# Kernel optimization log

Hardware: AMD Instinct MI355X
Metric: run time of the kernel (lower is better)

## Reference

```python
import jax, jax.numpy as jnp
import numpy as np

D_MODEL = 1024
N_HEADS = 2
D_FF = 4096
SEQ = 4096
HEAD_DIM = D_MODEL // N_HEADS
SCALE = HEAD_DIM ** 0.5
LN_EPS = 1e-5


def _layer_norm(x, g, b):
    mu = jnp.mean(x, axis=-1, keepdims=True)
    var = jnp.mean(jnp.square(x - mu), axis=-1, keepdims=True)
    return (x - mu) * jax.lax.rsqrt(var + LN_EPS) * g + b


def _gelu_tanh(x):
    # torch nn.GELU(approximate='tanh')
    c = np.sqrt(2.0 / np.pi).astype(np.float32)
    return 0.5 * x * (1.0 + jnp.tanh(c * (x + 0.044715 * x * x * x)))


def setup_inputs() -> dict:
    key = jax.random.key(0)
    ks = jax.random.split(key, 12)
    s = 1.0 / np.sqrt(D_MODEL)
    sf = 1.0 / np.sqrt(D_FF)
    inp = {
        "x": jax.random.normal(ks[0], (SEQ, D_MODEL), jnp.float32),
        "ln1_g": jnp.ones((D_MODEL,), jnp.float32),
        "ln1_b": jnp.zeros((D_MODEL,), jnp.float32),
        "wq": jax.random.normal(ks[1], (D_MODEL, D_MODEL), jnp.float32) * s,
        "bq": jnp.zeros((D_MODEL,), jnp.float32),
        "wk": jax.random.normal(ks[2], (D_MODEL, D_MODEL), jnp.float32) * s,
        "bk": jnp.zeros((D_MODEL,), jnp.float32),
        "wv": jax.random.normal(ks[3], (D_MODEL, D_MODEL), jnp.float32) * s,
        "bv": jnp.zeros((D_MODEL,), jnp.float32),
        "wo": jax.random.normal(ks[4], (D_MODEL, D_MODEL), jnp.float32) * s,
        "bo": jnp.zeros((D_MODEL,), jnp.float32),
        "ln2_g": jnp.ones((D_MODEL,), jnp.float32),
        "ln2_b": jnp.zeros((D_MODEL,), jnp.float32),
        "w1": jax.random.normal(ks[5], (D_FF, D_MODEL), jnp.float32) * s,
        "b1": jnp.zeros((D_FF,), jnp.float32),
        "w2": jax.random.normal(ks[6], (D_MODEL, D_FF), jnp.float32) * sf,
        "b2": jnp.zeros((D_MODEL,), jnp.float32),
    }
    return inp


def reference(x, ln1_g, ln1_b, wq, bq, wk, bk, wv, bv, wo, bo,
              ln2_g, ln2_b, w1, b1, w2, b2):
    S = x.shape[0]
    h = _layer_norm(x, ln1_g, ln1_b)
    # torch Linear: y = h @ W.T + b
    q = h @ wq.T + bq
    k = h @ wk.T + bk
    v = h @ wv.T + bv
    # chunk(2, dim=-1) == reshape last dim to (heads, head_dim)
    qh = q.reshape(S, N_HEADS, HEAD_DIM)
    kh = k.reshape(S, N_HEADS, HEAD_DIM)
    vh = v.reshape(S, N_HEADS, HEAD_DIM)
    scores = jnp.einsum('shd,thd->hst', qh, kh) / SCALE  # [H,S,S]
    attn = jax.nn.softmax(scores, axis=-1)
    o = jnp.einsum('hst,thd->shd', attn, vh).reshape(S, D_MODEL)
    x = x + (o @ wo.T + bo)
    h2 = _layer_norm(x, ln2_g, ln2_b)
    ff = _gelu_tanh(h2 @ w1.T + b1) @ w2.T + b2
    return x + ff
```

## Files before the change

kernel.cpp:

```cpp
#include <hip/hip_runtime.h>
#include <math.h>

#define SEQ 4096
#define DM  1024
#define DFF 4096
#define NH  2
#define HD  512

typedef unsigned short ushort_t;
typedef short  s16x8 __attribute__((ext_vector_type(8)));
typedef float  f32x4 __attribute__((ext_vector_type(4)));
typedef unsigned short u16x8 __attribute__((ext_vector_type(8)));

__device__ __forceinline__ float bf2f(unsigned short u) {
    return __uint_as_float(((unsigned)u) << 16);
}
__device__ __forceinline__ unsigned short f2bf(float f) {
    unsigned u = __float_as_uint(f);
    unsigned r = (u + 0x7fffu + ((u >> 16) & 1u)) >> 16;
    return (unsigned short)r;
}

__device__ __forceinline__ void async_load16(void* lds, const void* g) {
    __builtin_amdgcn_global_load_lds(
        (const __attribute__((address_space(1))) void*)g,
        (__attribute__((address_space(3))) void*)lds, 16, 0, 0);
}

template<bool HAS_BIAS, bool DO_GELU, bool HAS_RES, bool OUT_BF16, int SPLITS,
         int MODE, int BM, bool TRV>
__global__ __launch_bounds__(BM == 256 ? 512 : 256)
void gemm_nt(const ushort_t* __restrict__ A, int lda,
             const ushort_t* __restrict__ B, int ldb,
             void* __restrict__ Cv, int ldc,
             const float* __restrict__ bias,
             const float* __restrict__ res, int ldres,
             int K, float alpha,
             size_t strA, size_t strB, size_t strC, size_t strBias,
             float* __restrict__ rowsum, ushort_t* __restrict__ vt)
{
    __shared__ alignas(16) ushort_t sA[BM * 64];
    __shared__ alignas(16) ushort_t sB[128 * 64];

    const int z  = blockIdx.z;
    const int zb = z / SPLITS;
    const int ks = (z % SPLITS) * K;
    A += (size_t)zb * strA;
    B += (size_t)zb * strB;
    if (HAS_BIAS) bias += (size_t)zb * strBias;

    const int tid   = threadIdx.x;
    const int lane  = tid & 63;
    const int wave  = tid >> 6;
    const int waveM = wave >> 1, waveN = wave & 1;
    const int m0 = blockIdx.y * BM, n0 = blockIdx.x * 128;
    const int lr = lane & 15, quad = lane >> 4;

    f32x4 acc[4][4] = {};

    const ushort_t* Ag = A + (size_t)m0 * lda + ks;
    const ushort_t* Bg = B + (size_t)n0 * ldb + ks;

    const int ldRow = (lane >> 3);
    const int ldCol = (((lane & 7) ^ (lane >> 3)) * 8);
    const int NB = (BM == 256) ? 2 : 4;
    const int BW = (BM == 256) ? 16 : 32;

    for (int k0 = 0; k0 < K; k0 += 64) {
#pragma unroll
        for (int i = 0; i < 4; ++i) {
            int r = wave * 32 + i * 8 + ldRow;
            async_load16(&sA[(wave * 32 + i * 8) * 64],
                         Ag + (size_t)r * lda + k0 + ldCol);
        }
#pragma unroll
        for (int i = 0; i < NB; ++i) {
            int r = wave * BW + i * 8 + ldRow;
            async_load16(&sB[(wave * BW + i * 8) * 64],
                         Bg + (size_t)r * ldb + k0 + ldCol);
        }
        __syncthreads();

#pragma unroll
        for (int kk = 0; kk < 64; kk += 32) {
            const int pg = ((((kk >> 3) + quad) ^ (lr & 7)) << 3);
            s16x8 af[4], bfr[4];
#pragma unroll
            for (int mi = 0; mi < 4; ++mi)
                af[mi] = *(const s16x8*)&sA[(waveM * 64 + mi * 16 + lr) * 64 + pg];
#pragma unroll
            for (int ni = 0; ni < 4; ++ni)
                bfr[ni] = *(const s16x8*)&sB[(waveN * 64 + ni * 16 + lr) * 64 + pg];
#pragma unroll
            for (int mi = 0; mi < 4; ++mi)
#pragma unroll
                for (int ni = 0; ni < 4; ++ni)
                    acc[mi][ni] = __builtin_amdgcn_mfma_f32_16x16x32_bf16(
                        af[mi], bfr[ni], acc[mi][ni], 0, 0, 0);
        }
        __syncthreads();
    }

    if (TRV && zb == 2) {
#pragma unroll
        for (int mi = 0; mi < 4; ++mi) {
#pragma unroll
            for (int ni = 0; ni < 4; ++ni) {
                int t0 = m0 + waveM * 64 + mi * 16 + quad * 4;
                int col = n0 + waveN * 64 + ni * 16 + lr;
                unsigned b[4];
#pragma unroll
                for (int r = 0; r < 4; ++r) {
                    float v = acc[mi][ni][r] * alpha;
                    if (HAS_BIAS) v += bias[col];
                    b[r] = f2bf(v);
                }
                uint2 pk;
                pk.x = b[0] | (b[1] << 16);
                pk.y = b[2] | (b[3] << 16);
                int h = col >> 9, d = col & (HD - 1);
                *(uint2*)(vt + (size_t)h * HD * SEQ + (size_t)d * SEQ + t0) = pk;
            }
        }
        return;
    }

    float rs_part[4][4];
    if (MODE == 1) {
#pragma unroll
        for (int mi = 0; mi < 4; ++mi)
#pragma unroll
            for (int r = 0; r < 4; ++r) rs_part[mi][r] = 0.0f;
    }

#pragma unroll
    for (int mi = 0; mi < 4; ++mi) {
#pragma unroll
        for (int r = 0; r < 4; ++r) {
            int row = m0 + waveM * 64 + mi * 16 + quad * 4 + r;
#pragma unroll
            for (int ni = 0; ni < 4; ++ni) {
                int col = n0 + waveN * 64 + ni * 16 + lr;
                float v = acc[mi][ni][r] * alpha;
                if (HAS_BIAS) v += bias[col];
                if (DO_GELU) {
                    float xx = v;
                    float y2 = 1.5957691216057308f * (xx + 0.044715f * xx * xx * xx);
                    float t = __expf(y2);
                    v = xx * t / (t + 1.0f);
                }
                if (HAS_RES) v += res[(size_t)row * ldres + col];
                if (OUT_BF16) {
                    ushort_t bs = f2bf(MODE == 1 ? __expf(v) : v);
                    if (MODE == 1) rs_part[mi][r] += bf2f(bs);
                    ((ushort_t*)Cv)[(size_t)z * strC + (size_t)row * ldc + col] = bs;
                } else {
                    ((float*)Cv)[(size_t)z * strC + (size_t)row * ldc + col] = v;
                }
            }
        }
    }

    if (MODE == 1) {
#pragma unroll
        for (int mi = 0; mi < 4; ++mi) {
#pragma unroll
            for (int r = 0; r < 4; ++r) {
                float s = rs_part[mi][r];
                s += __shfl_xor(s, 1);
                s += __shfl_xor(s, 2);
                s += __shfl_xor(s, 4);
                s += __shfl_xor(s, 8);
                if (lr == 0) {
                    int row = m0 + waveM * 64 + mi * 16 + quad * 4 + r;
                    atomicAdd(&rowsum[(size_t)zb * SEQ + row], s);
                }
            }
        }
    }
}

template<int S, bool HAS_BIAS, bool HAS_RES, bool OUT_BF16, bool DIV_RS>
__global__ __launch_bounds__(256)
void reduce_splitk(const float* __restrict__ P, size_t slab,
                   void* __restrict__ outv, int N, int ldout, int colStride,
                   const float* __restrict__ bias,
                   const float* __restrict__ res, int ldres,
                   const float* __restrict__ rowsum)
{
    const int z = blockIdx.z;
    const float* Pz = P + (size_t)z * S * slab;
    size_t i = ((size_t)blockIdx.x * 256 + threadIdx.x) * 4;
    if (i >= slab) return;
    int row = (int)(i / (size_t)N);
    int col = (int)(i - (size_t)row * N);
    float4 a = *(const float4*)(Pz + i);
#pragma unroll
    for (int s = 1; s < S; ++s) {
        float4 b = *(const float4*)(Pz + (size_t)s * slab + i);
        a.x += b.x; a.y += b.y; a.z += b.z; a.w += b.w;
    }
    if (DIV_RS) {
        float inv = 1.0f / rowsum[(size_t)z * SEQ + row];
        a.x *= inv; a.y *= inv; a.z *= inv; a.w *= inv;
    }
    int oc = z * colStride + col;
    if (HAS_BIAS) {
        a.x += bias[oc]; a.y += bias[oc + 1]; a.z += bias[oc + 2]; a.w += bias[oc + 3];
    }
    if (HAS_RES) {
        float4 r4 = *(const float4*)(res + (size_t)row * ldres + oc);
        a.x += r4.x; a.y += r4.y; a.z += r4.z; a.w += r4.w;
    }
    if (OUT_BF16) {
        ushort_t* o = (ushort_t*)outv + (size_t)row * ldout + oc;
        o[0] = f2bf(a.x); o[1] = f2bf(a.y); o[2] = f2bf(a.z); o[3] = f2bf(a.w);
    } else {
        *(float4*)((float*)outv + (size_t)row * ldout + oc) = a;
    }
}

__global__ __launch_bounds__(256)
void reduce_oproj_ln(const float* __restrict__ P,
                     const float* __restrict__ bo, const float* __restrict__ x,
                     float* __restrict__ X1,
                     const float* __restrict__ g, const float* __restrict__ b,
                     ushort_t* __restrict__ H)
{
    int row = blockIdx.x;
    int tid = threadIdx.x;
    size_t off = (size_t)row * DM + tid * 4;
    float4 p0 = *(const float4*)(P + off);
    float4 p1 = *(const float4*)(P + (size_t)SEQ * DM + off);
    float4 bb = ((const float4*)bo)[tid];
    float4 xr = *(const float4*)(x + off);
    float4 v;
    v.x = p0.x + p1.x + bb.x + xr.x;
    v.y = p0.y + p1.y + bb.y + xr.y;
    v.z = p0.z + p1.z + bb.z + xr.z;
    v.w = p0.w + p1.w + bb.w + xr.w;
    *(float4*)(X1 + off) = v;

    float s1 = v.x + v.y + v.z + v.w;
    float s2 = v.x * v.x + v.y * v.y + v.z * v.z + v.w * v.w;
#pragma unroll
    for (int o = 32; o > 0; o >>= 1) {
        s1 += __shfl_down(s1, o);
        s2 += __shfl_down(s2, o);
    }
    __shared__ float r1[4], r2[4];
    if ((tid & 63) == 0) { r1[tid >> 6] = s1; r2[tid >> 6] = s2; }
    __syncthreads();
    s1 = r1[0] + r1[1] + r1[2] + r1[3];
    s2 = r2[0] + r2[1] + r2[2] + r2[3];
    float mu  = s1 * (1.0f / DM);
    float var = s2 * (1.0f / DM) - mu * mu;
    float rs  = rsqrtf(var + 1e-5f);
    float4 gg = ((const float4*)g)[tid];
    float4 be = ((const float4*)b)[tid];
    ushort_t* o = H + off;
    o[0] = f2bf((v.x - mu) * rs * gg.x + be.x);
    o[1] = f2bf((v.y - mu) * rs * gg.y + be.y);
    o[2] = f2bf((v.z - mu) * rs * gg.z + be.z);
    o[3] = f2bf((v.w - mu) * rs * gg.w + be.w);
}

__global__ __launch_bounds__(256)
void layernorm_kernel(const float* __restrict__ x, const float* __restrict__ g,
                      const float* __restrict__ b, ushort_t* __restrict__ out)
{
    int row = blockIdx.x;
    int tid = threadIdx.x;
    float4 v = ((const float4*)(x + (size_t)row * DM))[tid];
    float s1 = v.x + v.y + v.z + v.w;
    float s2 = v.x * v.x + v.y * v.y + v.z * v.z + v.w * v.w;
#pragma unroll
    for (int o = 32; o > 0; o >>= 1) {
        s1 += __shfl_down(s1, o);
        s2 += __shfl_down(s2, o);
    }
    __shared__ float r1[4], r2[4];
    if ((tid & 63) == 0) { r1[tid >> 6] = s1; r2[tid >> 6] = s2; }
    __syncthreads();
    s1 = r1[0] + r1[1] + r1[2] + r1[3];
    s2 = r2[0] + r2[1] + r2[2] + r2[3];
    float mu  = s1 * (1.0f / DM);
    float var = s2 * (1.0f / DM) - mu * mu;
    float rs  = rsqrtf(var + 1e-5f);
    float4 gg = ((const float4*)g)[tid];
    float4 bb = ((const float4*)b)[tid];
    ushort_t* o = out + (size_t)row * DM + tid * 4;
    o[0] = f2bf((v.x - mu) * rs * gg.x + bb.x);
    o[1] = f2bf((v.y - mu) * rs * gg.y + bb.y);
    o[2] = f2bf((v.z - mu) * rs * gg.z + bb.z);
    o[3] = f2bf((v.w - mu) * rs * gg.w + bb.w);
}

__global__ __launch_bounds__(256)
void prep_kernel(const float* __restrict__ wq, const float* __restrict__ wk,
                 const float* __restrict__ wv, const float* __restrict__ wo,
                 const float* __restrict__ w1, const float* __restrict__ w2,
                 ushort_t* __restrict__ WQ, ushort_t* __restrict__ WK,
                 ushort_t* __restrict__ WV, ushort_t* __restrict__ WO,
                 ushort_t* __restrict__ W1d, ushort_t* __restrict__ W2d,
                 const float* __restrict__ bq, const float* __restrict__ bk,
                 const float* __restrict__ bv, float* __restrict__ BQKV,
                 float* __restrict__ RSUM)
{
    const long S1   = (long)DM * DM / 4;
    const long SW   = 4 * S1;
    const long SBIG = (long)DFF * DM / 4;
    long i = (long)blockIdx.x * 256 + threadIdx.x;

    const float* src; ushort_t* dst; long off;
    if (i < SW) {
        long seg = i / S1; off = i - seg * S1;
        src = seg == 0 ? wq : seg == 1 ? wk : seg == 2 ? wv : wo;
        dst = seg == 0 ? WQ : seg == 1 ? WK : seg == 2 ? WV : WO;
    } else if (i < SW + SBIG) {
        off = i - SW; src = w1; dst = W1d;
    } else if (i < SW + 2 * SBIG) {
        off = i - SW - SBIG; src = w2; dst = W2d;
    } else {
        long j = i - (SW + 2 * SBIG);
        if (j < 3 * DM / 4) {
            long e = j * 4;
#pragma unroll
            for (int t = 0; t < 4; ++t) {
                long k = e + t;
                float v = k < DM ? bq[k] : k < 2 * DM ? bk[k - DM] : bv[k - 2 * DM];
                BQKV[k] = v;
            }
        } else if (j < 3 * DM / 4 + NH * SEQ / 4) {
            long k = (j - 3 * DM / 4) * 4;
            *(float4*)&RSUM[k] = make_float4(0.f, 0.f, 0.f, 0.f);
        }
        return;
    }
    float4 f = *(const float4*)(src + off * 4);
    ushort_t* d = dst + off * 4;
    d[0] = f2bf(f.x); d[1] = f2bf(f.y); d[2] = f2bf(f.z); d[3] = f2bf(f.w);
}

extern "C" void kernel_launch(void* const* d_in, const int* in_sizes, int n_in,
                              void* d_out, int out_size, void* d_ws, size_t ws_size,
                              hipStream_t stream)
{
    const float* x   = (const float*)d_in[0];
    const float* g1  = (const float*)d_in[1];
    const float* be1 = (const float*)d_in[2];
    const float* wq  = (const float*)d_in[3];
    const float* bq  = (const float*)d_in[4];
    const float* wk  = (const float*)d_in[5];
    const float* bk  = (const float*)d_in[6];
    const float* wv  = (const float*)d_in[7];
    const float* bv  = (const float*)d_in[8];
    const float* wo  = (const float*)d_in[9];
    const float* bo  = (const float*)d_in[10];
    const float* g2  = (const float*)d_in[11];
    const float* be2 = (const float*)d_in[12];
    const float* w1  = (const float*)d_in[13];
    const float* b1  = (const float*)d_in[14];
    const float* w2  = (const float*)d_in[15];
    const float* b2  = (const float*)d_in[16];
    float* out = (float*)d_out;

    char* ws = (char*)d_ws;
    const size_t MB = 1ull << 20;
    ushort_t* WQ   = (ushort_t*)(ws + 0 * MB);
    ushort_t* WK   = (ushort_t*)(ws + 2 * MB);
    ushort_t* WV   = (ushort_t*)(ws + 4 * MB);
    ushort_t* WO   = (ushort_t*)(ws + 6 * MB);
    ushort_t* W1   = (ushort_t*)(ws + 8 * MB);
    ushort_t* W2   = (ushort_t*)(ws + 16 * MB);
    ushort_t* H    = (ushort_t*)(ws + 24 * MB);
    ushort_t* Q    = (ushort_t*)(ws + 32 * MB);
    ushort_t* Kb   = (ushort_t*)(ws + 40 * MB);
    ushort_t* V    = (ushort_t*)(ws + 48 * MB);
    ushort_t* Vt   = (ushort_t*)(ws + 56 * MB);
    ushort_t* SC   = (ushort_t*)(ws + 64 * MB);
    ushort_t* O    = (ushort_t*)(ws + 128 * MB);
    float*    X1   = (float*)(ws + 136 * MB);
    float*    P    = (float*)(ws + 152 * MB);
    float*    BQKV = (float*)(ws + 216 * MB);
    float*    RSUM = (float*)(ws + 216 * MB + 16 * 1024);
    (void)V;

    dim3 blk(256), blk2(512);

    {
        long total = 4L * DM * DM + 2L * DFF * DM;
        long n4 = total / 4 + 3 * DM / 4 + NH * SEQ / 4;
        prep_kernel<<<dim3((unsigned)((n4 + 255) / 256)), blk, 0, stream>>>(
            wq, wk, wv, wo, w1, w2, WQ, WK, WV, WO, W1, W2,
            bq, bk, bv, BQKV, RSUM);
    }

    layernorm_kernel<<<SEQ, 256, 0, stream>>>(x, g1, be1, H);

    gemm_nt<true, false, false, true, 1, 0, 128, true>
        <<<dim3(DM / 128, SEQ / 128, 3), blk, 0, stream>>>(
        H, DM, WQ, DM, Q, DM, BQKV, nullptr, 0, DM, 1.0f,
        0, (size_t)DM * DM, (size_t)SEQ * DM, (size_t)DM, nullptr, Vt);

    const float scale = 0.044194173824159216f;
    gemm_nt<false, false, false, true, 1, 1, 256, false>
        <<<dim3(SEQ / 128, SEQ / 256, NH), blk2, 0, stream>>>(
        Q, DM, Kb, DM, SC, SEQ, nullptr, nullptr, 0, HD, scale,
        (size_t)HD, (size_t)HD, (size_t)SEQ * SEQ, 0, RSUM, nullptr);

    gemm_nt<false, false, false, false, 2, 0, 128, false>
        <<<dim3(HD / 128, SEQ / 128, NH * 2), blk, 0, stream>>>(
        SC, SEQ, Vt, SEQ, P, HD, nullptr, nullptr, 0, SEQ / 2, 1.0f,
        (size_t)SEQ * SEQ, (size_t)HD * SEQ, (size_t)SEQ * HD, 0, nullptr, nullptr);
    reduce_splitk<2, false, false, true, true>
        <<<dim3((SEQ * HD / 4) / 256, 1, NH), blk, 0, stream>>>(
        P, (size_t)SEQ * HD, O, HD, DM, HD, nullptr, nullptr, 0, RSUM);

    gemm_nt<false, false, false, false, 2, 0, 128, false>
        <<<dim3(DM / 128, SEQ / 128, 2), blk, 0, stream>>>(
        O, DM, WO, DM, P, DM, nullptr, nullptr, 0, DM / 2, 1.0f,
        0, 0, (size_t)SEQ * DM, 0, nullptr, nullptr);
    reduce_oproj_ln<<<SEQ, 256, 0, stream>>>(P, bo, x, X1, g2, be2, H);

    ushort_t* F1 = SC;
    gemm_nt<true, true, false, true, 1, 0, 256, false>
        <<<dim3(DFF / 128, SEQ / 256, 1), blk2, 0, stream>>>(
        H, DM, W1, DM, F1, DFF, b1, nullptr, 0, DM, 1.0f, 0, 0, 0, 0,
        nullptr, nullptr);

    gemm_nt<false, false, false, false, 2, 0, 128, false>
        <<<dim3(DM / 128, SEQ / 128, 2), blk, 0, stream>>>(
        F1, DFF, W2, DFF, P, DM, nullptr, nullptr, 0, DFF / 2, 1.0f,
        0, 0, (size_t)SEQ * DM, 0, nullptr, nullptr);
    reduce_splitk<2, true, true, false, false>
        <<<dim3((SEQ * DM / 4) / 256, 1, 1), blk, 0, stream>>>(
        P, (size_t)SEQ * DM, out, DM, DM, 0, b2, X1, DM, nullptr);
}
```

Before: 415.1 us.

## Switch GEMM to 32x32x16 MFMA tiles, fuse LayerNorm into prep, enlarge QKV tile

Replaces the 16x16x32 bf16 MFMA inner loop with 32x32x16 MFMAs on 2x2 accumulators per wave, so fewer LDS fragment loads are needed per FLOP, and remaps all epilogues (V transpose, exp/rowsum, general) to the 32x32 output layout. The first LayerNorm is folded into the weight-conversion prep kernel to remove one launch. The QKV GEMM now uses the 256-row tile with 512 threads. The new output layout changes the store and shuffle patterns and may affect coalescing and register pressure.

```diff
diff --git a/kernel.cpp b/kernel.cpp
--- a/kernel.cpp
+++ b/kernel.cpp
@@ -8,9 +8,8 @@
 #define HD  512
 
 typedef unsigned short ushort_t;
-typedef short  s16x8 __attribute__((ext_vector_type(8)));
-typedef float  f32x4 __attribute__((ext_vector_type(4)));
-typedef unsigned short u16x8 __attribute__((ext_vector_type(8)));
+typedef short  s16x8  __attribute__((ext_vector_type(8)));
+typedef float  f32x16 __attribute__((ext_vector_type(16)));
 
 __device__ __forceinline__ float bf2f(unsigned short u) {
     return __uint_as_float(((unsigned)u) << 16);
@@ -54,9 +53,9 @@
     const int wave  = tid >> 6;
     const int waveM = wave >> 1, waveN = wave & 1;
     const int m0 = blockIdx.y * BM, n0 = blockIdx.x * 128;
-    const int lr = lane & 15, quad = lane >> 4;
-
-    f32x4 acc[4][4] = {};
+    const int lr32 = lane & 31, half = lane >> 5;
+
+    f32x16 acc[2][2] = {};
 
     const ushort_t* Ag = A + (size_t)m0 * lda + ks;
     const ushort_t* Bg = B + (size_t)n0 * ldb + ks;
@@ -69,33 +68,31 @@
     for (int k0 = 0; k0 < K; k0 += 64) {
 #pragma unroll
         for (int i = 0; i < 4; ++i) {
-            int r = wave * 32 + i * 8 + ldRow;
             async_load16(&sA[(wave * 32 + i * 8) * 64],
-                         Ag + (size_t)r * lda + k0 + ldCol);
+                         Ag + (size_t)(wave * 32 + i * 8 + ldRow) * lda + k0 + ldCol);
         }
 #pragma unroll
         for (int i = 0; i < NB; ++i) {
-            int r = wave * BW + i * 8 + ldRow;
             async_load16(&sB[(wave * BW + i * 8) * 64],
-                         Bg + (size_t)r * ldb + k0 + ldCol);
+                         Bg + (size_t)(wave * BW + i * 8 + ldRow) * ldb + k0 + ldCol);
         }
         __syncthreads();
 
 #pragma unroll
-        for (int kk = 0; kk < 64; kk += 32) {
-            const int pg = ((((kk >> 3) + quad) ^ (lr & 7)) << 3);
-            s16x8 af[4], bfr[4];
-#pragma unroll
-            for (int mi = 0; mi < 4; ++mi)
-                af[mi] = *(const s16x8*)&sA[(waveM * 64 + mi * 16 + lr) * 64 + pg];
-#pragma unroll
-            for (int ni = 0; ni < 4; ++ni)
-                bfr[ni] = *(const s16x8*)&sB[(waveN * 64 + ni * 16 + lr) * 64 + pg];
-#pragma unroll
-            for (int mi = 0; mi < 4; ++mi)
-#pragma unroll
-                for (int ni = 0; ni < 4; ++ni)
-                    acc[mi][ni] = __builtin_amdgcn_mfma_f32_16x16x32_bf16(
+        for (int kk = 0; kk < 64; kk += 16) {
+            const int px = (((kk >> 3) + half) ^ (lr32 & 7)) << 3;
+            s16x8 af[2], bfr[2];
+#pragma unroll
+            for (int mi = 0; mi < 2; ++mi)
+                af[mi] = *(const s16x8*)&sA[(waveM * 64 + mi * 32 + lr32) * 64 + px];
+#pragma unroll
+            for (int ni = 0; ni < 2; ++ni)
+                bfr[ni] = *(const s16x8*)&sB[(waveN * 64 + ni * 32 + lr32) * 64 + px];
+#pragma unroll
+            for (int mi = 0; mi < 2; ++mi)
+#pragma unroll
+                for (int ni = 0; ni < 2; ++ni)
+                    acc[mi][ni] = __builtin_amdgcn_mfma_f32_32x32x16_bf16(
                         af[mi], bfr[ni], acc[mi][ni], 0, 0, 0);
         }
         __syncthreads();
@@ -103,46 +100,66 @@
 
     if (TRV && zb == 2) {
 #pragma unroll
-        for (int mi = 0; mi < 4; ++mi) {
-#pragma unroll
-            for (int ni = 0; ni < 4; ++ni) {
-                int t0 = m0 + waveM * 64 + mi * 16 + quad * 4;
-                int col = n0 + waveN * 64 + ni * 16 + lr;
-                unsigned b[4];
-#pragma unroll
-                for (int r = 0; r < 4; ++r) {
+        for (int mi = 0; mi < 2; ++mi) {
+#pragma unroll
+            for (int ni = 0; ni < 2; ++ni) {
+                int col = n0 + waveN * 64 + ni * 32 + lr32;
+                float bval = HAS_BIAS ? bias[col] : 0.0f;
+                int h = col >> 9, d = col & (HD - 1);
+#pragma unroll
+                for (int g = 0; g < 4; ++g) {
+                    int t0 = m0 + waveM * 64 + mi * 32 + 8 * g + 4 * half;
+                    unsigned b[4];
+#pragma unroll
+                    for (int j = 0; j < 4; ++j)
+                        b[j] = f2bf(acc[mi][ni][4 * g + j] * alpha + bval);
+                    uint2 pk;
+                    pk.x = b[0] | (b[1] << 16);
+                    pk.y = b[2] | (b[3] << 16);
+                    *(uint2*)(vt + (size_t)h * HD * SEQ + (size_t)d * SEQ + t0) = pk;
+                }
+            }
+        }
+        return;
+    }
+
+    if (MODE == 1) {
+#pragma unroll
+        for (int mi = 0; mi < 2; ++mi) {
+#pragma unroll
+            for (int r = 0; r < 16; ++r) {
+                int row = m0 + waveM * 64 + mi * 32 + (r & 3) + 8 * (r >> 2) + 4 * half;
+                float s = 0.0f;
+#pragma unroll
+                for (int ni = 0; ni < 2; ++ni) {
+                    int col = n0 + waveN * 64 + ni * 32 + lr32;
                     float v = acc[mi][ni][r] * alpha;
-                    if (HAS_BIAS) v += bias[col];
-                    b[r] = f2bf(v);
+                    ushort_t bs = f2bf(__expf(v));
+                    s += bf2f(bs);
+                    ((ushort_t*)Cv)[(size_t)z * strC + (size_t)row * ldc + col] = bs;
                 }
-                uint2 pk;
-                pk.x = b[0] | (b[1] << 16);
-                pk.y = b[2] | (b[3] << 16);
-                int h = col >> 9, d = col & (HD - 1);
-                *(uint2*)(vt + (size_t)h * HD * SEQ + (size_t)d * SEQ + t0) = pk;
+                s += __shfl_xor(s, 1);
+                s += __shfl_xor(s, 2);
+                s += __shfl_xor(s, 4);
+                s += __shfl_xor(s, 8);
+                s += __shfl_xor(s, 16);
+                if (lr32 == 0)
+                    atomicAdd(&rowsum[(size_t)zb * SEQ + row], s);
             }
         }
         return;
     }
 
-    float rs_part[4][4];
-    if (MODE == 1) {
-#pragma unroll
-        for (int mi = 0; mi < 4; ++mi)
-#pragma unroll
-            for (int r = 0; r < 4; ++r) rs_part[mi][r] = 0.0f;
-    }
-
-#pragma unroll
-    for (int mi = 0; mi < 4; ++mi) {
-#pragma unroll
-        for (int r = 0; r < 4; ++r) {
-            int row = m0 + waveM * 64 + mi * 16 + quad * 4 + r;
-#pragma unroll
-            for (int ni = 0; ni < 4; ++ni) {
-                int col = n0 + waveN * 64 + ni * 16 + lr;
-                float v = acc[mi][ni][r] * alpha;
-                if (HAS_BIAS) v += bias[col];
+#pragma unroll
+    for (int mi = 0; mi < 2; ++mi) {
+#pragma unroll
+        for (int ni = 0; ni < 2; ++ni) {
+            int col = n0 + waveN * 64 + ni * 32 + lr32;
+            float bval = HAS_BIAS ? bias[col] : 0.0f;
+#pragma unroll
+            for (int r = 0; r < 16; ++r) {
+                int row = m0 + waveM * 64 + mi * 32 + (r & 3) + 8 * (r >> 2) + 4 * half;
+                float v = acc[mi][ni][r] * alpha + bval;
                 if (DO_GELU) {
                     float xx = v;
                     float y2 = 1.5957691216057308f * (xx + 0.044715f * xx * xx * xx);
@@ -150,31 +167,10 @@
                     v = xx * t / (t + 1.0f);
                 }
                 if (HAS_RES) v += res[(size_t)row * ldres + col];
-                if (OUT_BF16) {
-                    ushort_t bs = f2bf(MODE == 1 ? __expf(v) : v);
-                    if (MODE == 1) rs_part[mi][r] += bf2f(bs);
-                    ((ushort_t*)Cv)[(size_t)z * strC + (size_t)row * ldc + col] = bs;
-                } else {
+                if (OUT_BF16)
+                    ((ushort_t*)Cv)[(size_t)z * strC + (size_t)row * ldc + col] = f2bf(v);
+                else
                     ((float*)Cv)[(size_t)z * strC + (size_t)row * ldc + col] = v;
-                }
-            }
-        }
-    }
-
-    if (MODE == 1) {
-#pragma unroll
-        for (int mi = 0; mi < 4; ++mi) {
-#pragma unroll
-            for (int r = 0; r < 4; ++r) {
-                float s = rs_part[mi][r];
-                s += __shfl_xor(s, 1);
-                s += __shfl_xor(s, 2);
-                s += __shfl_xor(s, 4);
-                s += __shfl_xor(s, 8);
-                if (lr == 0) {
-                    int row = m0 + waveM * 64 + mi * 16 + quad * 4 + r;
-                    atomicAdd(&rowsum[(size_t)zb * SEQ + row], s);
-                }
             }
         }
     }
@@ -266,51 +262,51 @@
 }
 
 __global__ __launch_bounds__(256)
-void layernorm_kernel(const float* __restrict__ x, const float* __restrict__ g,
-                      const float* __restrict__ b, ushort_t* __restrict__ out)
+void prep_ln(const float* __restrict__ wq, const float* __restrict__ wk,
+             const float* __restrict__ wv, const float* __restrict__ wo,
+             const float* __restrict__ w1, const float* __restrict__ w2,
+             ushort_t* __restrict__ WQ, ushort_t* __restrict__ WK,
+             ushort_t* __restrict__ WV, ushort_t* __restrict__ WO,
+             ushort_t* __restrict__ W1d, ushort_t* __restrict__ W2d,
+             const float* __restrict__ bq, const float* __restrict__ bk,
+             const float* __restrict__ bv, float* __restrict__ BQKV,
+             float* __restrict__ RSUM,
+             const float* __restrict__ x, const float* __restrict__ g1,
+             const float* __restrict__ be1, ushort_t* __restrict__ H)
 {
-    int row = blockIdx.x;
     int tid = threadIdx.x;
-    float4 v = ((const float4*)(x + (size_t)row * DM))[tid];
-    float s1 = v.x + v.y + v.z + v.w;
-    float s2 = v.x * v.x + v.y * v.y + v.z * v.z + v.w * v.w;
-#pragma unroll
-    for (int o = 32; o > 0; o >>= 1) {
-        s1 += __shfl_down(s1, o);
-        s2 += __shfl_down(s2, o);
-    }
-    __shared__ float r1[4], r2[4];
-    if ((tid & 63) == 0) { r1[tid >> 6] = s1; r2[tid >> 6] = s2; }
-    __syncthreads();
-    s1 = r1[0] + r1[1] + r1[2] + r1[3];
-    s2 = r2[0] + r2[1] + r2[2] + r2[3];
-    float mu  = s1 * (1.0f / DM);
-    float var = s2 * (1.0f / DM) - mu * mu;
-    float rs  = rsqrtf(var + 1e-5f);
-    float4 gg = ((const float4*)g)[tid];
-    float4 bb = ((const float4*)b)[tid];
-    ushort_t* o = out + (size_t)row * DM + tid * 4;
-    o[0] = f2bf((v.x - mu) * rs * gg.x + bb.x);
-    o[1] = f2bf((v.y - mu) * rs * gg.y + bb.y);
-    o[2] = f2bf((v.z - mu) * rs * gg.z + bb.z);
-    o[3] = f2bf((v.w - mu) * rs * gg.w + bb.w);
-}
-
-__global__ __launch_bounds__(256)
-void prep_kernel(const float* __restrict__ wq, const float* __restrict__ wk,
-                 const float* __restrict__ wv, const float* __restrict__ wo,
-                 const float* __restrict__ w1, const float* __restrict__ w2,
-                 ushort_t* __restrict__ WQ, ushort_t* __restrict__ WK,
-                 ushort_t* __restrict__ WV, ushort_t* __restrict__ WO,
-                 ushort_t* __restrict__ W1d, ushort_t* __restrict__ W2d,
-                 const float* __restrict__ bq, const float* __restrict__ bk,
-                 const float* __restrict__ bv, float* __restrict__ BQKV,
-                 float* __restrict__ RSUM)
-{
+    if (blockIdx.x < SEQ) {
+        int row = blockIdx.x;
+        float4 v = ((const float4*)(x + (size_t)row * DM))[tid];
+        float s1 = v.x + v.y + v.z + v.w;
+        float s2 = v.x * v.x + v.y * v.y + v.z * v.z + v.w * v.w;
+#pragma unroll
+        for (int o = 32; o > 0; o >>= 1) {
+            s1 += __shfl_down(s1, o);
+            s2 += __shfl_down(s2, o);
+        }
+        __shared__ float r1[4], r2[4];
+        if ((tid & 63) == 0) { r1[tid >> 6] = s1; r2[tid >> 6] = s2; }
+        __syncthreads();
+        s1 = r1[0] + r1[1] + r1[2] + r1[3];
+        s2 = r2[0] + r2[1] + r2[2] + r2[3];
+        float mu  = s1 * (1.0f / DM);
+        float var = s2 * (1.0f / DM) - mu * mu;
+        float rs  = rsqrtf(var + 1e-5f);
+        float4 gg = ((const float4*)g1)[tid];
+        float4 bb = ((const float4*)be1)[tid];
+        ushort_t* o = H + (size_t)row * DM + tid * 4;
+        o[0] = f2bf((v.x - mu) * rs * gg.x + bb.x);
+        o[1] = f2bf((v.y - mu) * rs * gg.y + bb.y);
+        o[2] = f2bf((v.z - mu) * rs * gg.z + bb.z);
+        o[3] = f2bf((v.w - mu) * rs * gg.w + bb.w);
+        return;
+    }
+
     const long S1   = (long)DM * DM / 4;
     const long SW   = 4 * S1;
     const long SBIG = (long)DFF * DM / 4;
-    long i = (long)blockIdx.x * 256 + threadIdx.x;
+    long i = (long)(blockIdx.x - SEQ) * 256 + tid;
 
     const float* src; ushort_t* dst; long off;
     if (i < SW) {
@@ -376,7 +372,6 @@
     ushort_t* H    = (ushort_t*)(ws + 24 * MB);
     ushort_t* Q    = (ushort_t*)(ws + 32 * MB);
     ushort_t* Kb   = (ushort_t*)(ws + 40 * MB);
-    ushort_t* V    = (ushort_t*)(ws + 48 * MB);
     ushort_t* Vt   = (ushort_t*)(ws + 56 * MB);
     ushort_t* SC   = (ushort_t*)(ws + 64 * MB);
     ushort_t* O    = (ushort_t*)(ws + 128 * MB);
@@ -384,22 +379,20 @@
     float*    P    = (float*)(ws + 152 * MB);
     float*    BQKV = (float*)(ws + 216 * MB);
     float*    RSUM = (float*)(ws + 216 * MB + 16 * 1024);
-    (void)V;
 
     dim3 blk(256), blk2(512);
 
     {
         long total = 4L * DM * DM + 2L * DFF * DM;
         long n4 = total / 4 + 3 * DM / 4 + NH * SEQ / 4;
-        prep_kernel<<<dim3((unsigned)((n4 + 255) / 256)), blk, 0, stream>>>(
+        unsigned prepBlocks = (unsigned)((n4 + 255) / 256);
+        prep_ln<<<dim3(SEQ + prepBlocks), blk, 0, stream>>>(
             wq, wk, wv, wo, w1, w2, WQ, WK, WV, WO, W1, W2,
-            bq, bk, bv, BQKV, RSUM);
-    }
-
-    layernorm_kernel<<<SEQ, 256, 0, stream>>>(x, g1, be1, H);
-
-    gemm_nt<true, false, false, true, 1, 0, 128, true>
-        <<<dim3(DM / 128, SEQ / 128, 3), blk, 0, stream>>>(
+            bq, bk, bv, BQKV, RSUM, x, g1, be1, H);
+    }
+
+    gemm_nt<true, false, false, true, 1, 0, 256, true>
+        <<<dim3(DM / 128, SEQ / 256, 3), blk2, 0, stream>>>(
         H, DM, WQ, DM, Q, DM, BQKV, nullptr, 0, DM, 1.0f,
         0, (size_t)DM * DM, (size_t)SEQ * DM, (size_t)DM, nullptr, Vt);
 
```

Result: slower. 424.3 us (+2.2%).
